# Kernel optimization log

Hardware: AMD Instinct MI355X
Metric: run time of the kernel (lower is better)

## Reference

```python
import jax, jax.numpy as jnp
import numpy as np

B, N, DIM, K = 4, 4096, 128, 16


def setup_inputs() -> dict:
    key = jax.random.key(0)
    ks = jax.random.split(key, 20)
    s = 0.05
    inp = {
        "x": jax.random.normal(ks[0], (B, N, DIM), jnp.float32),
        "pos": jax.random.normal(ks[1], (B, N, 3), jnp.float32),
        # pos_mlp: Linear(3,dim) -> ReLU -> Linear(dim,dim)
        "pw1": jax.random.normal(ks[2], (3, DIM), jnp.float32) * s,
        "pb1": jnp.zeros((DIM,), jnp.float32),
        "pw2": jax.random.normal(ks[3], (DIM, DIM), jnp.float32) * s,
        "pb2": jnp.zeros((DIM,), jnp.float32),
        # q/k/v projections
        "qw": jax.random.normal(ks[4], (DIM, DIM), jnp.float32) * s,
        "qb": jnp.zeros((DIM,), jnp.float32),
        "kw": jax.random.normal(ks[5], (DIM, DIM), jnp.float32) * s,
        "kb": jnp.zeros((DIM,), jnp.float32),
        "vw": jax.random.normal(ks[6], (DIM, DIM), jnp.float32) * s,
        "vb": jnp.zeros((DIM,), jnp.float32),
        # attn MLP: Linear(dim, dim//4) -> ReLU -> Linear(dim//4, dim)
        "aw1": jax.random.normal(ks[7], (DIM, DIM // 4), jnp.float32) * s,
        "ab1": jnp.zeros((DIM // 4,), jnp.float32),
        "aw2": jax.random.normal(ks[8], (DIM // 4, DIM), jnp.float32) * s,
        "ab2": jnp.zeros((DIM,), jnp.float32),
    }
    return inp


def reference(x, pos, pw1, pb1, pw2, pb2, qw, qb, kw, kb, vw, vb, aw1, ab1, aw2, ab2):
    Bs, Np, C = x.shape
    k = K
    # pairwise squared distances: |pi|^2 + |pj|^2 - 2 pi.pj  -> (B,N,N)
    inner = jnp.einsum('bnd,bmd->bnm', pos, pos)
    xx = jnp.sum(pos * pos, axis=2, keepdims=True)  # (B,N,1)
    dist = xx + jnp.swapaxes(xx, 1, 2) - 2.0 * inner
    # k nearest neighbors (smallest dist) -> indices (B,N,k)
    _, idx = jax.lax.top_k(-dist, k)
    bidx = jnp.arange(Bs)[:, None, None]
    neighbors = x[bidx, idx]        # (B,N,k,C)
    pos_neighbors = pos[bidx, idx]  # (B,N,k,3)
    pos_relative = pos[:, :, None, :] - pos_neighbors  # (B,N,k,3)
    # pos MLP
    pe = jax.nn.relu(pos_relative @ pw1 + pb1) @ pw2 + pb2  # (B,N,k,C)
    q = (x @ qw + qb)[:, :, None, :]   # (B,N,1,C)
    kk = neighbors @ kw + kb           # (B,N,k,C)
    v = neighbors @ vw + vb            # (B,N,k,C)
    a = q - kk + pe
    attn = jax.nn.relu(a @ aw1 + ab1) @ aw2 + ab2  # (B,N,k,C)
    attn = jax.nn.softmax(attn, axis=2)
    out = jnp.sum(attn * (v + pe), axis=2)  # (B,N,C)
    return out
```

## Files before the change

kernel.cpp:

```cpp
#include <hip/hip_runtime.h>
#include <hip/hip_bf16.h>
#include <stdint.h>

#define BATCH 4
#define NPTS  4096
#define DIM   128
#define KNN   16
#define NROWS (BATCH*NPTS)
#define NCHUNK 16
#define CHUNK  (NPTS/NCHUNK)

typedef unsigned long long u64;
typedef unsigned int u32;
typedef unsigned short u16;
typedef __attribute__((ext_vector_type(8))) short short8;
typedef __attribute__((ext_vector_type(4))) float f32x4;

__device__ __forceinline__ u16 f2bf(float f) {
  u32 u = __float_as_uint(f);
  u += 0x7FFFu + ((u >> 16) & 1);
  return (u16)(u >> 16);
}

__global__ __launch_bounds__(256) void prep_pos4(const float* __restrict__ pos,
                                                 float4* __restrict__ pos4) {
  int i = blockIdx.x * 256 + threadIdx.x;
  if (i < NROWS) pos4[i] = make_float4(pos[3*i], pos[3*i+1], pos[3*i+2], 0.f);
}

__global__ __launch_bounds__(256) void prep_matmul(
    const float* __restrict__ pw2, const float* __restrict__ qw, const float* __restrict__ kw,
    const float* __restrict__ aw1,
    u16* __restrict__ w1T, float* __restrict__ Wq2, float* __restrict__ Wk2) {
  int p = blockIdx.x >> 2, qtr = blockIdx.x & 3;
  const float* A = p == 0 ? pw2 : (p == 1 ? qw : kw);
  int j = threadIdx.x & 31;
  int r0 = qtr*32 + (threadIdx.x >> 5)*4;
  float acc[4] = {0.f,0.f,0.f,0.f};
  for (int c = 0; c < 128; ++c) {
    float av = aw1[c*32 + j];
#pragma unroll
    for (int rr = 0; rr < 4; ++rr) acc[rr] = fmaf(A[(r0+rr)*128 + c], av, acc[rr]);
  }
#pragma unroll
  for (int rr = 0; rr < 4; ++rr) {
    int h = r0 + rr;
    if (p == 0)      w1T[j*128 + (h ^ ((j&7)<<3))] = f2bf(acc[rr]);
    else if (p == 1) Wq2[h*32 + j] = acc[rr];
    else             Wk2[h*32 + j] = acc[rr];
  }
}

__global__ __launch_bounds__(256) void prep_convert(
    const float* __restrict__ pw2, const float* __restrict__ aw2,
    const float* __restrict__ pw1, const float* __restrict__ pb1,
    const float* __restrict__ qb, const float* __restrict__ kb,
    const float* __restrict__ pb2, const float* __restrict__ aw1, const float* __restrict__ ab1,
    u16* __restrict__ pw2T, u16* __restrict__ aw2T,
    float4* __restrict__ pw1q, float* __restrict__ bias1) {
  int bid = blockIdx.x, tid = threadIdx.x;
  if (bid < 64) {
    int e = bid*256 + tid; int k = e >> 7, n = e & 127;
    pw2T[n*128 + (k ^ ((n&7)<<3))] = f2bf(pw2[k*128 + n]);
  } else if (bid < 80) {
    int e = (bid-64)*256 + tid; int k = e >> 7, n = e & 127;
    aw2T[n*32 + (k ^ ((n&3)<<3))] = f2bf(aw2[k*128 + n]);
  } else {
    if (tid < 128) {
      int c = tid;
      pw1q[c ^ ((c & 0x18) >> 2)] = make_float4(pw1[c], pw1[128+c], pw1[256+c], pb1[c]);
    } else if (tid < 160) {
      int j = tid - 128;
      float s = ab1[j];
      for (int c = 0; c < 128; ++c) s += (qb[c]-kb[c]+pb2[c]) * aw1[c*32+j];
      bias1[j] = s;
    }
  }
}

template <typename T>
__device__ __forceinline__ void cex(T& a, T& b) {
  T mn = a < b ? a : b;
  T mx = a < b ? b : a;
  a = mn; b = mx;
}
template <typename T>
__device__ __forceinline__ void sort16(T x[16]) {
#pragma unroll
  for (int k = 2; k <= 16; k <<= 1)
#pragma unroll
    for (int j = k >> 1; j > 0; j >>= 1)
#pragma unroll
      for (int i = 0; i < 16; ++i) {
        int l = i ^ j;
        if (l > i) { if ((i & k) == 0) cex(x[i], x[l]); else cex(x[l], x[i]); }
      }
}
template <typename T>
__device__ __forceinline__ void merge16(T A[16], const T B[16]) {
#pragma unroll
  for (int i = 0; i < 16; ++i) { T b = B[15 - i]; A[i] = A[i] < b ? A[i] : b; }
#pragma unroll
  for (int j = 8; j > 0; j >>= 1)
#pragma unroll
    for (int i = 0; i < 16; ++i) { int l = i ^ j; if (l > i) cex(A[i], A[l]); }
}
__device__ __forceinline__ void bmerge32(u32 x[32]) {
#pragma unroll
  for (int j = 16; j > 0; j >>= 1)
#pragma unroll
    for (int i = 0; i < 32; ++i) { int l = i ^ j; if (l > i) cex(x[i], x[l]); }
}

__global__ __launch_bounds__(256) void knn_scan(const float4* __restrict__ pos4,
                                                u32* __restrict__ part) {
  __shared__ float4 cs[4][CHUNK];
  const int lane  = threadIdx.x & 63;
  const int w     = threadIdx.x >> 6;
  const int task  = blockIdx.x * 4 + w;
  const int qg    = task >> 4;
  const int chunk = task & 15;
  const int qbase = qg * 64;
  const int b     = qbase >> 12;
  const int cbase = chunk * CHUNK;

  const float4* cand = pos4 + b*NPTS + cbase;
#pragma unroll
  for (int i = 0; i < CHUNK/64; ++i) cs[w][lane + 64*i] = cand[lane + 64*i];
  __syncthreads();

  float4 qp = pos4[qbase + lane];
  const float qx = qp.x, qy = qp.y, qz = qp.z;

  u32 best[16];
#pragma unroll
  for (int i = 0; i < 16; ++i) best[i] = ~0u;

#pragma unroll 1
  for (int m = 0; m < CHUNK/16; ++m) {
    u32 batch[16];
#pragma unroll
    for (int e = 0; e < 16; ++e) {
      float4 p = cs[w][m*16 + e];
      float dx = qx - p.x, dy = qy - p.y, dz = qz - p.z;
      float d  = fmaf(dx, dx, fmaf(dy, dy, dz*dz));
      batch[e] = (__float_as_uint(d) & 0xFFFFF000u) | (u32)(cbase + m*16 + e);
    }
    sort16(batch);
    merge16(best, batch);
  }
  const int q = qbase + lane;
  uint4* dst = (uint4*)(part + q*256 + chunk*16);
#pragma unroll
  for (int t = 0; t < 4; ++t)
    dst[t] = make_uint4(best[4*t], best[4*t+1], best[4*t+2], best[4*t+3]);
}

__global__ __launch_bounds__(256) void knn_refine(const float4* __restrict__ pos4,
                                                  const u32* __restrict__ part,
                                                  int* __restrict__ knnIdx) {
  __shared__ u64 A64[16][137];
  __shared__ u32 Bu[16][264];
  u32 (*Au)[274] = (u32 (*)[274])A64;

  const int tid = threadIdx.x;
  const int qi = tid >> 4, c = tid & 15;
  const int q  = blockIdx.x * 16 + qi;
  const int b  = q >> 12;

  {
    const uint4* src = (const uint4*)(part + q*256 + c*16);
    u32 own[16];
#pragma unroll
    for (int t = 0; t < 4; ++t) {
      uint4 v = src[t];
      own[4*t+0]=v.x; own[4*t+1]=v.y; own[4*t+2]=v.z; own[4*t+3]=v.w;
    }
#pragma unroll
    for (int s = 0; s < 16; ++s) Au[qi][c*17 + s] = own[s];
  }
  __syncthreads();

  if (c < 8) {
    u32 x[32];
#pragma unroll
    for (int s = 0; s < 16; ++s) x[s]      = Au[qi][(2*c)*17 + s];
#pragma unroll
    for (int s = 0; s < 16; ++s) x[16 + s] = Au[qi][(2*c+1)*17 + 15 - s];
    bmerge32(x);
#pragma unroll
    for (int s = 0; s < 32; ++s) Bu[qi][c*33 + s] = x[s];
  }
  __syncthreads();

  if (c < 4) {
    u32 x[32];
#pragma unroll
    for (int s = 0; s < 32; ++s) {
      u32 a = Bu[qi][(2*c)*33 + s], bb = Bu[qi][(2*c+1)*33 + 31 - s];
      x[s] = a < bb ? a : bb;
    }
    bmerge32(x);
#pragma unroll
    for (int s = 0; s < 32; ++s) Au[qi][c*33 + s] = x[s];
  }
  __syncthreads();

  if (c < 2) {
    u32 x[32];
#pragma unroll
    for (int s = 0; s < 32; ++s) {
      u32 a = Au[qi][(2*c)*33 + s], bb = Au[qi][(2*c+1)*33 + 31 - s];
      x[s] = a < bb ? a : bb;
    }
    bmerge32(x);
#pragma unroll
    for (int s = 0; s < 32; ++s) Bu[qi][c*33 + s] = x[s];
  }
  __syncthreads();

  if (c == 0) {
    u32 x[32];
#pragma unroll
    for (int s = 0; s < 32; ++s) {
      u32 a = Bu[qi][s], bb = Bu[qi][33 + 31 - s];
      x[s] = a < bb ? a : bb;
    }
    bmerge32(x);
#pragma unroll
    for (int s = 0; s < 32; ++s) Bu[qi][132 + s] = x[s];
  }
  __syncthreads();

  if (c < 2) {
    float4 qp = pos4[q];
    const double qx = qp.x, qy = qp.y, qz = qp.z;
    u64 key[16];
#pragma unroll
    for (int s = 0; s < 16; ++s) {
      int idx = (int)(Bu[qi][132 + c*16 + s] & 0xFFFu);
      float4 p = pos4[(b<<12) + idx];
      double dx = qx - (double)p.x;
      double dy = qy - (double)p.y;
      double dz = qz - (double)p.z;
      double d  = fma(dx, dx, fma(dy, dy, dz*dz));
      key[s] = (((u64)__double_as_longlong(d)) & ~0xFFFull) | (u64)idx;
    }
    sort16(key);
#pragma unroll
    for (int s = 0; s < 16; ++s) A64[qi][c*17 + s] = key[s];
  }
  __syncthreads();

  if (c == 0) {
    u64 best[16], nb[16];
#pragma unroll
    for (int s = 0; s < 16; ++s) { best[s] = A64[qi][s]; nb[s] = A64[qi][17 + s]; }
    merge16(best, nb);
    const int outq = q * KNN;
#pragma unroll
    for (int s = 0; s < 16; ++s) knnIdx[outq + s] = (int)(best[s] & 0xFFFull);
  }
}

__global__ __launch_bounds__(256) void proj_v(
    const float* __restrict__ x,
    const float* __restrict__ vw, const float* __restrict__ vb,
    const float* __restrict__ Wq2, const float* __restrict__ Wk2,
    float* __restrict__ vo, float* __restrict__ qa, float* __restrict__ ka) {
  __shared__ float xs[32*DIM];
  const int row0 = blockIdx.x * 32;
  const int tid = threadIdx.x;
  {
    const float4* src = (const float4*)(x + row0*DIM);
    float4* dst = (float4*)xs;
#pragma unroll
    for (int i = 0; i < 4; ++i) dst[tid + 256*i] = src[tid + 256*i];
  }
  __syncthreads();
  {
    const int c = tid & 127, g2 = tid >> 7;
    float av[16];
#pragma unroll
    for (int r = 0; r < 16; ++r) av[r] = 0.f;
    for (int d4 = 0; d4 < 32; ++d4) {
      float wv[4];
#pragma unroll
      for (int t = 0; t < 4; ++t) wv[t] = vw[(d4*4+t)*DIM + c];
#pragma unroll
      for (int r = 0; r < 16; ++r) {
        float4 xv = *(const float4*)&xs[(g2*16+r)*DIM + d4*4];
        av[r] = fmaf(xv.x, wv[0], av[r]);
        av[r] = fmaf(xv.y, wv[1], av[r]);
        av[r] = fmaf(xv.z, wv[2], av[r]);
        av[r] = fmaf(xv.w, wv[3], av[r]);
      }
    }
    float bv = vb[c];
#pragma unroll
    for (int r = 0; r < 16; ++r) vo[(row0 + g2*16 + r)*DIM + c] = av[r] + bv;
  }
  {
    const int j = tid & 31, grp = tid >> 5;
    float aq[4] = {0.f,0.f,0.f,0.f}, ak[4] = {0.f,0.f,0.f,0.f};
    for (int d4 = 0; d4 < 32; ++d4) {
#pragma unroll
      for (int t = 0; t < 4; ++t) {
        int d = d4*4 + t;
        float wq = Wq2[d*32 + j], wk = Wk2[d*32 + j];
#pragma unroll
        for (int rr = 0; rr < 4; ++rr) {
          float xv = xs[(grp*4+rr)*DIM + d];
          aq[rr] = fmaf(xv, wq, aq[rr]);
          ak[rr] = fmaf(xv, wk, ak[rr]);
        }
      }
    }
#pragma unroll
    for (int rr = 0; rr < 4; ++rr) {
      qa[(row0 + grp*4 + rr)*32 + j] = aq[rr];
      ka[(row0 + grp*4 + rr)*32 + j] = ak[rr];
    }
  }
}

__global__ __launch_bounds__(256) void attn_mfma(
    const float4* __restrict__ pos4, const int* __restrict__ knnIdx,
    const float* __restrict__ vws, const float* __restrict__ qa, const float* __restrict__ ka,
    const u16* __restrict__ pw2T, const u16* __restrict__ w1T, const u16* __restrict__ aw2T,
    const float4* __restrict__ pw1q, const float* __restrict__ bias1,
    const float* __restrict__ pb2, const float* __restrict__ ab2,
    float* __restrict__ out) {
  __shared__ __align__(16) u16 pw2s[16384];
  __shared__ __align__(16) u16 w1s[4096];
  __shared__ __align__(16) u16 aw2s[4096];
  __shared__ __align__(16) float4 pw1s[128];
  __shared__ float bias1s[32];
  __shared__ float pb2s[128];
  __shared__ float ab2s[128];
  __shared__ __align__(16) u16 h2t[4][512];
  __shared__ float4 rels[4][16];
  __shared__ int ids[4][16];

  const int tid = threadIdx.x;
  {
    const uint4* s1 = (const uint4*)pw2T; uint4* d1 = (uint4*)pw2s;
#pragma unroll
    for (int i = 0; i < 8; ++i) d1[tid + 256*i] = s1[tid + 256*i];
    const uint4* s2 = (const uint4*)w1T; uint4* d2 = (uint4*)w1s;
#pragma unroll
    for (int i = 0; i < 2; ++i) d2[tid + 256*i] = s2[tid + 256*i];
    const uint4* s3 = (const uint4*)aw2T; uint4* d3 = (uint4*)aw2s;
#pragma unroll
    for (int i = 0; i < 2; ++i) d3[tid + 256*i] = s3[tid + 256*i];
    if (tid < 128) { pw1s[tid] = pw1q[tid]; pb2s[tid] = pb2[tid]; ab2s[tid] = ab2[tid]; }
    else if (tid < 160) bias1s[tid-128] = bias1[tid-128];
  }
  __syncthreads();

  const int lane = tid & 63, w = tid >> 6;
  const int c16 = lane & 15, g = lane >> 4;

  for (int it = 0; it < 4; ++it) {
    const int q = blockIdx.x*16 + w*4 + it;
    const int b = q >> 12;
    if (lane < 16) {
      int id = knnIdx[q*KNN + lane];
      ids[w][lane] = id;
      float4 pq = pos4[q], pn = pos4[(b<<12) + id];
      rels[w][lane] = make_float4(pq.x-pn.x, pq.y-pn.y, pq.z-pn.z, 0.f);
    }
    __syncthreads();

    int idr[4];
#pragma unroll
    for (int r = 0; r < 4; ++r) idr[r] = ids[w][g*4 + r];

    float qa_v[2], ka_v[2][4];
#pragma unroll
    for (int t = 0; t < 2; ++t) qa_v[t] = qa[q*32 + t*16 + c16];
#pragma unroll
    for (int r = 0; r < 4; ++r)
#pragma unroll
      for (int t = 0; t < 2; ++t) ka_v[t][r] = ka[((b<<12)+idr[r])*32 + t*16 + c16];

    float4 rl = rels[w][c16];
    short8 h1f[4];
#pragma unroll
    for (int kc = 0; kc < 4; ++kc) {
      short8 s;
#pragma unroll
      for (int j = 0; j < 8; ++j) {
        int c = kc*32 + g*8 + j;
        float4 wv = pw1s[c ^ ((c & 0x18) >> 2)];
        float h = fmaf(rl.x, wv.x, fmaf(rl.y, wv.y, fmaf(rl.z, wv.z, wv.w)));
        s[j] = (short)f2bf(fmaxf(h, 0.f));
      }
      h1f[kc] = s;
    }

    f32x4 pe[8];
#pragma unroll
    for (int nt = 0; nt < 8; ++nt) { f32x4 z = {0.f,0.f,0.f,0.f}; pe[nt] = z; }
#pragma unroll
    for (int kc = 0; kc < 4; ++kc)
#pragma unroll
      for (int nt = 0; nt < 8; ++nt) {
        int n = nt*16 + c16;
        short8 bf = *(const short8*)&pw2s[n*128 + ((kc*32 + g*8) ^ ((n&7)<<3))];
        pe[nt] = __builtin_amdgcn_mfma_f32_16x16x32_bf16(h1f[kc], bf, pe[nt], 0, 0, 0);
      }

    f32x4 ha[2];
#pragma unroll
    for (int t = 0; t < 2; ++t) { f32x4 z = {0.f,0.f,0.f,0.f}; ha[t] = z; }
#pragma unroll
    for (int kc = 0; kc < 4; ++kc)
#pragma unroll
      for (int t = 0; t < 2; ++t) {
        int n = t*16 + c16;
        short8 bf = *(const short8*)&w1s[n*128 + ((kc*32 + g*8) ^ ((n&7)<<3))];
        ha[t] = __builtin_amdgcn_mfma_f32_16x16x32_bf16(h1f[kc], bf, ha[t], 0, 0, 0);
      }

#pragma unroll
    for (int t = 0; t < 2; ++t)
#pragma unroll
      for (int r = 0; r < 4; ++r) {
        float v = ha[t][r] + qa_v[t] - ka_v[t][r] + bias1s[t*16 + c16];
        int row = g*4 + r, col = t*16 + c16;
        h2t[w][row*32 + (col ^ ((row&3)<<3))] = f2bf(fmaxf(v, 0.f));
      }
    __syncthreads();

    short8 h2f = *(const short8*)&h2t[w][c16*32 + ((g*8) ^ ((c16&3)<<3))];

    f32x4 lg[8];
#pragma unroll
    for (int nt = 0; nt < 8; ++nt) {
      int n = nt*16 + c16;
      float ab = ab2s[n];
      f32x4 cini = {ab, ab, ab, ab};
      short8 bf = *(const short8*)&aw2s[n*32 + ((g*8) ^ ((n&3)<<3))];
      lg[nt] = __builtin_amdgcn_mfma_f32_16x16x32_bf16(h2f, bf, cini, 0, 0, 0);
    }

    float vv[8][4];
#pragma unroll
    for (int r = 0; r < 4; ++r) {
      const float* vrow = vws + (size_t)((b<<12) + idr[r])*DIM;
#pragma unroll
      for (int nt = 0; nt < 8; ++nt) vv[nt][r] = vrow[nt*16 + c16];
    }

#pragma unroll
    for (int nt = 0; nt < 8; ++nt) {
      float m = fmaxf(fmaxf(lg[nt][0], lg[nt][1]), fmaxf(lg[nt][2], lg[nt][3]));
      m = fmaxf(m, __shfl_xor(m, 16));
      m = fmaxf(m, __shfl_xor(m, 32));
      float e0 = __expf(lg[nt][0]-m), e1 = __expf(lg[nt][1]-m),
            e2 = __expf(lg[nt][2]-m), e3 = __expf(lg[nt][3]-m);
      float s = e0+e1+e2+e3;
      s += __shfl_xor(s, 16);
      s += __shfl_xor(s, 32);
      float inv = 1.0f / s;
      float pb = pb2s[nt*16 + c16];
      float acc = e0*(vv[nt][0] + pe[nt][0] + pb)
                + e1*(vv[nt][1] + pe[nt][1] + pb)
                + e2*(vv[nt][2] + pe[nt][2] + pb)
                + e3*(vv[nt][3] + pe[nt][3] + pb);
      acc *= inv;
      acc += __shfl_xor(acc, 16);
      acc += __shfl_xor(acc, 32);
      if (lane < 16) out[q*DIM + nt*16 + lane] = acc;
    }
  }
}

extern "C" void kernel_launch(void* const* d_in, const int* in_sizes, int n_in,
                              void* d_out, int out_size, void* d_ws, size_t ws_size,
                              hipStream_t stream) {
  const float* x   = (const float*)d_in[0];
  const float* pos = (const float*)d_in[1];
  const float* pw1 = (const float*)d_in[2];
  const float* pb1 = (const float*)d_in[3];
  const float* pw2 = (const float*)d_in[4];
  const float* pb2 = (const float*)d_in[5];
  const float* qw  = (const float*)d_in[6];
  const float* qb  = (const float*)d_in[7];
  const float* kw  = (const float*)d_in[8];
  const float* kb  = (const float*)d_in[9];
  const float* vw  = (const float*)d_in[10];
  const float* vb  = (const float*)d_in[11];
  const float* aw1 = (const float*)d_in[12];
  const float* ab1 = (const float*)d_in[13];
  const float* aw2 = (const float*)d_in[14];
  const float* ab2 = (const float*)d_in[15];
  float* out = (float*)d_out;

  char* ws = (char*)d_ws;
  float4* pos4   = (float4*)(ws);
  int*    knnIdx = (int*)(ws + (1u<<20));
  u32*    part   = (u32*)(ws + (2u<<20));
  float*  vws    = (float*)(ws + (2u<<20));
  float*  qa     = (float*)(ws + (11u<<20));
  float*  ka     = (float*)(ws + (13u<<20));
  char*   wsw    = ws + (19u<<20);
  u16*    pw2T  = (u16*)(wsw);
  u16*    w1T   = (u16*)(wsw + 32768);
  u16*    aw2T  = (u16*)(wsw + 40960);
  float4* pw1q  = (float4*)(wsw + 49152);
  float*  bias1 = (float*)(wsw + 51200);
  float*  Wq2   = (float*)(wsw + 51328);
  float*  Wk2   = (float*)(wsw + 67712);

  prep_pos4<<<NROWS/256, 256, 0, stream>>>(pos, pos4);
  prep_matmul<<<12, 256, 0, stream>>>(pw2, qw, kw, aw1, w1T, Wq2, Wk2);
  prep_convert<<<81, 256, 0, stream>>>(pw2, aw2, pw1, pb1, qb, kb, pb2, aw1, ab1,
                                       pw2T, aw2T, pw1q, bias1);
  knn_scan<<<(NROWS/64)*NCHUNK/4, 256, 0, stream>>>(pos4, part);
  knn_refine<<<NROWS/16, 256, 0, stream>>>(pos4, part, knnIdx);
  proj_v<<<NROWS/32, 256, 0, stream>>>(x, vw, vb, Wq2, Wk2, vws, qa, ka);
  attn_mfma<<<NROWS/16, 256, 0, stream>>>(pos4, knnIdx, vws, qa, ka,
                                          pw2T, w1T, aw2T, pw1q, bias1, pb2, ab2, out);
}
```

Measured before the change: 251.8 us.

## Enlarge attention blocks to 16 waves, use wave-local LDS fences, swizzle blocks

```diff
diff --git a/kernel.cpp b/kernel.cpp
--- a/kernel.cpp
+++ b/kernel.cpp
@@ -21,6 +21,8 @@
   u += 0x7FFFu + ((u >> 16) & 1);
   return (u16)(u >> 16);
 }
+
+#define WAVE_LDS_FENCE() asm volatile("s_waitcnt lgkmcnt(0)" ::: "memory")
 
 __global__ __launch_bounds__(256) void prep_pos4(const float* __restrict__ pos,
                                                  float4* __restrict__ pos4) {
@@ -324,7 +326,8 @@
   }
 }
 
-__global__ __launch_bounds__(256) void attn_mfma(
+#define AW 16
+__global__ __launch_bounds__(1024, 4) void attn_mfma(
     const float4* __restrict__ pos4, const int* __restrict__ knnIdx,
     const float* __restrict__ vws, const float* __restrict__ qa, const float* __restrict__ ka,
     const u16* __restrict__ pw2T, const u16* __restrict__ w1T, const u16* __restrict__ aw2T,
@@ -338,21 +341,17 @@
   __shared__ float bias1s[32];
   __shared__ float pb2s[128];
   __shared__ float ab2s[128];
-  __shared__ __align__(16) u16 h2t[4][512];
-  __shared__ float4 rels[4][16];
-  __shared__ int ids[4][16];
+  __shared__ __align__(16) u16 h2t[AW][512];
+  __shared__ float4 rels[AW][16];
+  __shared__ int ids[AW][16];
 
   const int tid = threadIdx.x;
   {
     const uint4* s1 = (const uint4*)pw2T; uint4* d1 = (uint4*)pw2s;
-#pragma unroll
-    for (int i = 0; i < 8; ++i) d1[tid + 256*i] = s1[tid + 256*i];
-    const uint4* s2 = (const uint4*)w1T; uint4* d2 = (uint4*)w1s;
-#pragma unroll
-    for (int i = 0; i < 2; ++i) d2[tid + 256*i] = s2[tid + 256*i];
-    const uint4* s3 = (const uint4*)aw2T; uint4* d3 = (uint4*)aw2s;
-#pragma unroll
-    for (int i = 0; i < 2; ++i) d3[tid + 256*i] = s3[tid + 256*i];
+    d1[tid] = s1[tid];
+    d1[tid + 1024] = s1[tid + 1024];
+    if (tid < 512)       ((uint4*)w1s)[tid]        = ((const uint4*)w1T)[tid];
+    else if (tid < 1024) ((uint4*)aw2s)[tid - 512] = ((const uint4*)aw2T)[tid - 512];
     if (tid < 128) { pw1s[tid] = pw1q[tid]; pb2s[tid] = pb2[tid]; ab2s[tid] = ab2[tid]; }
     else if (tid < 160) bias1s[tid-128] = bias1[tid-128];
   }
@@ -360,9 +359,11 @@
 
   const int lane = tid & 63, w = tid >> 6;
   const int c16 = lane & 15, g = lane >> 4;
+  const int swz = (blockIdx.x & 7) * 32 + (blockIdx.x >> 3);
+  const int qbase = swz * 64 + w * 4;
 
   for (int it = 0; it < 4; ++it) {
-    const int q = blockIdx.x*16 + w*4 + it;
+    const int q = qbase + it;
     const int b = q >> 12;
     if (lane < 16) {
       int id = knnIdx[q*KNN + lane];
@@ -370,7 +371,7 @@
       float4 pq = pos4[q], pn = pos4[(b<<12) + id];
       rels[w][lane] = make_float4(pq.x-pn.x, pq.y-pn.y, pq.z-pn.z, 0.f);
     }
-    __syncthreads();
+    WAVE_LDS_FENCE();
 
     int idr[4];
 #pragma unroll
@@ -431,7 +432,7 @@
         int row = g*4 + r, col = t*16 + c16;
         h2t[w][row*32 + (col ^ ((row&3)<<3))] = f2bf(fmaxf(v, 0.f));
       }
-    __syncthreads();
+    WAVE_LDS_FENCE();
 
     short8 h2f = *(const short8*)&h2t[w][c16*32 + ((g*8) ^ ((c16&3)<<3))];
 
@@ -521,6 +522,6 @@
   knn_scan<<<(NROWS/64)*NCHUNK/4, 256, 0, stream>>>(pos4, part);
   knn_refine<<<NROWS/16, 256, 0, stream>>>(pos4, part, knnIdx);
   proj_v<<<NROWS/32, 256, 0, stream>>>(x, vw, vb, Wq2, Wk2, vws, qa, ka);
-  attn_mfma<<<NROWS/16, 256, 0, stream>>>(pos4, knnIdx, vws, qa, ka,
-                                          pw2T, w1T, aw2T, pw1q, bias1, pb2, ab2, out);
-}
+  attn_mfma<<<NROWS/64, 1024, 0, stream>>>(pos4, knnIdx, vws, qa, ka,
+                                           pw2T, w1T, aw2T, pw1q, bias1, pb2, ab2, out);
+}
```

Result: slower. 266.5 us (+5.9%).
